# Performance work log

Measured on AMD Instinct MI355X. Metric: run time of the kernel, lower is better.

## Reference

```python
import jax, jax.numpy as jnp
import numpy as np

B, P, PLOIDY = 8, 5000, 2
NALLELES, NPOS, D = 16, 20000, 64


def setup_inputs() -> dict:
    key = jax.random.key(0)
    k1, k2, k3, k4, k5 = jax.random.split(key, 5)
    alleles = jax.random.randint(k1, (B, P, PLOIDY), 0, NALLELES, dtype=jnp.int32)
    positions = jax.random.randint(k2, (B, P), 0, NPOS, dtype=jnp.int32)
    allele_table = jax.random.normal(k3, (NALLELES, D), dtype=jnp.float32)
    kernel_table = jax.random.normal(k4, (NPOS, D * D), dtype=jnp.float32)
    bias_table = jax.random.normal(k5, (NPOS, D), dtype=jnp.float32)
    return {"alleles": alleles, "positions": positions,
            "allele_table": allele_table, "kernel_table": kernel_table,
            "bias_table": bias_table}


def reference(alleles, positions, allele_table, kernel_table, bias_table):
    # gather allele embeddings and sum over ploidy: [B,P,ploidy,D] -> [B,P,D]
    a = allele_table[alleles].sum(axis=-2)
    # per-position weight matrix: [B,P,D,D]
    kernel = kernel_table[positions].reshape(positions.shape[0], positions.shape[1], D, D)
    bias = bias_table[positions]                       # [B,P,D]
    # batched 1xD @ DxD matmul, fused with bias add
    out = jnp.einsum('bpd,bpde->bpe', a, kernel) + bias
    return out  # activation is None (linear)
```

## Files before the change

kernel.cpp:

```cpp
#include <hip/hip_runtime.h>

#define BB 8
#define PP 5000
#define DD 64
#define NBP (BB * PP)
#define NPOSC 20000
#define WAVES_PER_BLOCK 4
#define GRID_MAIN (NBP / WAVES_PER_BLOCK)

#define BSHIFT 4
#define NBUCKET 1250
#define NBUCKET_PAD 1280

__global__ __launch_bounds__(256) void hist_kernel(
    const int* __restrict__ positions, int* __restrict__ hist)
{
    const int tid = blockIdx.x * 256 + threadIdx.x;
    if (tid < NBP) atomicAdd(&hist[positions[tid] >> BSHIFT], 1);
}

__global__ __launch_bounds__(256) void scan_kernel(
    const int* __restrict__ hist, int* __restrict__ offs)
{
    __shared__ int lsum[256];
    const int t = threadIdx.x;
    const int base = t * 5;
    int v[5];
#pragma unroll
    for (int j = 0; j < 5; ++j)
        v[j] = (base + j < NBUCKET) ? hist[base + j] : 0;
    int run = 0;
#pragma unroll
    for (int j = 0; j < 5; ++j) { int x = v[j]; v[j] = run; run += x; }
    lsum[t] = run;
    __syncthreads();
    if (t == 0) {
        int acc = 0;
        for (int i = 0; i < 256; ++i) { int x = lsum[i]; lsum[i] = acc; acc += x; }
    }
    __syncthreads();
#pragma unroll
    for (int j = 0; j < 5; ++j)
        if (base + j < NBUCKET) offs[base + j] = lsum[t] + v[j];
}

__global__ __launch_bounds__(256) void scatter_kernel(
    const int* __restrict__ positions, int* __restrict__ offs,
    int* __restrict__ order)
{
    const int tid = blockIdx.x * 256 + threadIdx.x;
    if (tid < NBP) {
        const int b = positions[tid] >> BSHIFT;
        const int idx = atomicAdd(&offs[b], 1);
        order[idx] = tid;
    }
}

__global__ __launch_bounds__(256) void allele_embed_kernel(
    const int* __restrict__ alleles,
    const int* __restrict__ positions,
    const float* __restrict__ allele_table,
    const float4* __restrict__ ktab4,
    const float4* __restrict__ btab4,
    const int* __restrict__ order,
    float4* __restrict__ out4)
{
    const int wave = threadIdx.x >> 6;
    const int lane = threadIdx.x & 63;
    const int work = (blockIdx.x & 7) * (GRID_MAIN / 8) + (blockIdx.x >> 3);
    const int bp   = order[work * WAVES_PER_BLOCK + wave];

    const int al0 = alleles[bp * 2 + 0];
    const int al1 = alleles[bp * 2 + 1];
    const int pos = positions[bp];

    const float a_full = allele_table[al0 * DD + lane] + allele_table[al1 * DD + lane];

    const float4* __restrict__ krow = ktab4 + (size_t)pos * (DD * DD / 4);
    const int dg = lane >> 4;

    float4 acc = make_float4(0.f, 0.f, 0.f, 0.f);
#pragma unroll
    for (int i = 0; i < 16; ++i) {
        const int d    = i * 4 + dg;
        const float ad = __shfl(a_full, d, 64);
        const float4 kv = krow[i * 64 + lane];
        acc.x += ad * kv.x;
        acc.y += ad * kv.y;
        acc.z += ad * kv.z;
        acc.w += ad * kv.w;
    }

#pragma unroll
    for (int off = 16; off <= 32; off <<= 1) {
        acc.x += __shfl_xor(acc.x, off, 64);
        acc.y += __shfl_xor(acc.y, off, 64);
        acc.z += __shfl_xor(acc.z, off, 64);
        acc.w += __shfl_xor(acc.w, off, 64);
    }

    if (lane < 16) {
        const float4 bv = btab4[(size_t)pos * (DD / 4) + lane];
        acc.x += bv.x;
        acc.y += bv.y;
        acc.z += bv.z;
        acc.w += bv.w;
        out4[(size_t)bp * (DD / 4) + lane] = acc;
    }
}

extern "C" void kernel_launch(void* const* d_in, const int* in_sizes, int n_in,
                              void* d_out, int out_size, void* d_ws, size_t ws_size,
                              hipStream_t stream) {
    const int*   alleles      = (const int*)d_in[0];
    const int*   positions    = (const int*)d_in[1];
    const float* allele_table = (const float*)d_in[2];
    const float4* ktab4       = (const float4*)d_in[3];
    const float4* btab4       = (const float4*)d_in[4];
    float4* out4              = (float4*)d_out;

    int* hist  = (int*)d_ws;
    int* offs  = hist + NBUCKET_PAD;
    int* order = offs + NBUCKET_PAD;

    hipMemsetAsync(hist, 0, NBUCKET_PAD * sizeof(int), stream);

    const int gprep = (NBP + 255) / 256;
    hist_kernel<<<gprep, 256, 0, stream>>>(positions, hist);
    scan_kernel<<<1, 256, 0, stream>>>(hist, offs);
    scatter_kernel<<<gprep, 256, 0, stream>>>(positions, offs, order);

    allele_embed_kernel<<<GRID_MAIN, WAVES_PER_BLOCK * 64, 0, stream>>>(
        alleles, positions, allele_table, ktab4, btab4, order, out4);
}
```

Baseline: 452.4 us.

## Group items by exact position and reuse each kernel row across all its items

Measured after the change: 499.2 us. 1.1x slower.

```diff
diff --git a/kernel.cpp b/kernel.cpp
--- a/kernel.cpp
+++ b/kernel.cpp
@@ -5,107 +5,134 @@
 #define DD 64
 #define NBP (BB * PP)
 #define NPOSC 20000
-#define WAVES_PER_BLOCK 4
-#define GRID_MAIN (NBP / WAVES_PER_BLOCK)
+#define GRID_POS (NPOSC / 4)
+#define CHUNK 80
 
-#define BSHIFT 4
-#define NBUCKET 1250
-#define NBUCKET_PAD 1280
+static __device__ __forceinline__ float4 f4add(float4 a, float4 b) {
+    return make_float4(a.x + b.x, a.y + b.y, a.z + b.z, a.w + b.w);
+}
 
 __global__ __launch_bounds__(256) void hist_kernel(
     const int* __restrict__ positions, int* __restrict__ hist)
 {
     const int tid = blockIdx.x * 256 + threadIdx.x;
-    if (tid < NBP) atomicAdd(&hist[positions[tid] >> BSHIFT], 1);
+    if (tid < NBP) atomicAdd(&hist[positions[tid]], 1);
 }
 
 __global__ __launch_bounds__(256) void scan_kernel(
-    const int* __restrict__ hist, int* __restrict__ offs)
+    const int* __restrict__ hist, int* __restrict__ offs,
+    int* __restrict__ cursor)
 {
     __shared__ int lsum[256];
     const int t = threadIdx.x;
-    const int base = t * 5;
-    int v[5];
-#pragma unroll
-    for (int j = 0; j < 5; ++j)
-        v[j] = (base + j < NBUCKET) ? hist[base + j] : 0;
+    const int base = t * CHUNK;
     int run = 0;
-#pragma unroll
-    for (int j = 0; j < 5; ++j) { int x = v[j]; v[j] = run; run += x; }
+    for (int j = 0; j < CHUNK; ++j) {
+        const int idx = base + j;
+        if (idx < NPOSC) run += hist[idx];
+    }
     lsum[t] = run;
     __syncthreads();
     if (t == 0) {
         int acc = 0;
-        for (int i = 0; i < 256; ++i) { int x = lsum[i]; lsum[i] = acc; acc += x; }
+        for (int i = 0; i < 256; ++i) { const int x = lsum[i]; lsum[i] = acc; acc += x; }
     }
     __syncthreads();
-#pragma unroll
-    for (int j = 0; j < 5; ++j)
-        if (base + j < NBUCKET) offs[base + j] = lsum[t] + v[j];
+    int acc = lsum[t];
+    for (int j = 0; j < CHUNK; ++j) {
+        const int idx = base + j;
+        if (idx < NPOSC) {
+            offs[idx]   = acc;
+            cursor[idx] = acc;
+            acc += hist[idx];
+        }
+    }
+    if (t == 255) offs[NPOSC] = acc;
 }
 
 __global__ __launch_bounds__(256) void scatter_kernel(
-    const int* __restrict__ positions, int* __restrict__ offs,
+    const int* __restrict__ positions, int* __restrict__ cursor,
     int* __restrict__ order)
 {
     const int tid = blockIdx.x * 256 + threadIdx.x;
     if (tid < NBP) {
-        const int b = positions[tid] >> BSHIFT;
-        const int idx = atomicAdd(&offs[b], 1);
+        const int idx = atomicAdd(&cursor[positions[tid]], 1);
         order[idx] = tid;
     }
 }
 
 __global__ __launch_bounds__(256) void allele_embed_kernel(
     const int* __restrict__ alleles,
-    const int* __restrict__ positions,
     const float* __restrict__ allele_table,
     const float4* __restrict__ ktab4,
     const float4* __restrict__ btab4,
+    const int* __restrict__ offs,
     const int* __restrict__ order,
     float4* __restrict__ out4)
 {
     const int wave = threadIdx.x >> 6;
     const int lane = threadIdx.x & 63;
-    const int work = (blockIdx.x & 7) * (GRID_MAIN / 8) + (blockIdx.x >> 3);
-    const int bp   = order[work * WAVES_PER_BLOCK + wave];
+    const int work = (blockIdx.x & 7) * (GRID_POS / 8) + (blockIdx.x >> 3);
+    const int pos  = work * 4 + wave;
 
-    const int al0 = alleles[bp * 2 + 0];
-    const int al1 = alleles[bp * 2 + 1];
-    const int pos = positions[bp];
-
-    const float a_full = allele_table[al0 * DD + lane] + allele_table[al1 * DD + lane];
+    const int start = offs[pos];
+    const int end   = offs[pos + 1];
+    if (start == end) return;
 
     const float4* __restrict__ krow = ktab4 + (size_t)pos * (DD * DD / 4);
     const int dg = lane >> 4;
+    const float4 bv = btab4[(size_t)pos * (DD / 4) + (lane & 15)];
 
-    float4 acc = make_float4(0.f, 0.f, 0.f, 0.f);
+    for (int c = start; c < end; c += 4) {
+        const int m = end - c;
+        const int bp0 = order[c];
+        const int bp1 = (m > 1) ? order[c + 1] : bp0;
+        const int bp2 = (m > 2) ? order[c + 2] : bp0;
+        const int bp3 = (m > 3) ? order[c + 3] : bp0;
+
+        const float a0 = allele_table[alleles[bp0 * 2] * DD + lane]
+                       + allele_table[alleles[bp0 * 2 + 1] * DD + lane];
+        const float a1 = allele_table[alleles[bp1 * 2] * DD + lane]
+                       + allele_table[alleles[bp1 * 2 + 1] * DD + lane];
+        const float a2 = allele_table[alleles[bp2 * 2] * DD + lane]
+                       + allele_table[alleles[bp2 * 2 + 1] * DD + lane];
+        const float a3 = allele_table[alleles[bp3 * 2] * DD + lane]
+                       + allele_table[alleles[bp3 * 2 + 1] * DD + lane];
+
+        float4 acc0 = make_float4(0.f, 0.f, 0.f, 0.f);
+        float4 acc1 = acc0, acc2 = acc0, acc3 = acc0;
 #pragma unroll
-    for (int i = 0; i < 16; ++i) {
-        const int d    = i * 4 + dg;
-        const float ad = __shfl(a_full, d, 64);
-        const float4 kv = krow[i * 64 + lane];
-        acc.x += ad * kv.x;
-        acc.y += ad * kv.y;
-        acc.z += ad * kv.z;
-        acc.w += ad * kv.w;
-    }
+        for (int i = 0; i < 16; ++i) {
+            const int d = i * 4 + dg;
+            const float4 kv = krow[i * 64 + lane];
+            const float d0 = __shfl(a0, d, 64);
+            const float d1 = __shfl(a1, d, 64);
+            const float d2 = __shfl(a2, d, 64);
+            const float d3 = __shfl(a3, d, 64);
+            acc0.x += d0 * kv.x; acc0.y += d0 * kv.y; acc0.z += d0 * kv.z; acc0.w += d0 * kv.w;
+            acc1.x += d1 * kv.x; acc1.y += d1 * kv.y; acc1.z += d1 * kv.z; acc1.w += d1 * kv.w;
+            acc2.x += d2 * kv.x; acc2.y += d2 * kv.y; acc2.z += d2 * kv.z; acc2.w += d2 * kv.w;
+            acc3.x += d3 * kv.x; acc3.y += d3 * kv.y; acc3.z += d3 * kv.z; acc3.w += d3 * kv.w;
+        }
 
 #pragma unroll
-    for (int off = 16; off <= 32; off <<= 1) {
-        acc.x += __shfl_xor(acc.x, off, 64);
-        acc.y += __shfl_xor(acc.y, off, 64);
-        acc.z += __shfl_xor(acc.z, off, 64);
-        acc.w += __shfl_xor(acc.w, off, 64);
-    }
+        for (int off = 16; off <= 32; off <<= 1) {
+            acc0.x += __shfl_xor(acc0.x, off, 64); acc0.y += __shfl_xor(acc0.y, off, 64);
+            acc0.z += __shfl_xor(acc0.z, off, 64); acc0.w += __shfl_xor(acc0.w, off, 64);
+            acc1.x += __shfl_xor(acc1.x, off, 64); acc1.y += __shfl_xor(acc1.y, off, 64);
+            acc1.z += __shfl_xor(acc1.z, off, 64); acc1.w += __shfl_xor(acc1.w, off, 64);
+            acc2.x += __shfl_xor(acc2.x, off, 64); acc2.y += __shfl_xor(acc2.y, off, 64);
+            acc2.z += __shfl_xor(acc2.z, off, 64); acc2.w += __shfl_xor(acc2.w, off, 64);
+            acc3.x += __shfl_xor(acc3.x, off, 64); acc3.y += __shfl_xor(acc3.y, off, 64);
+            acc3.z += __shfl_xor(acc3.z, off, 64); acc3.w += __shfl_xor(acc3.w, off, 64);
+        }
 
-    if (lane < 16) {
-        const float4 bv = btab4[(size_t)pos * (DD / 4) + lane];
-        acc.x += bv.x;
-        acc.y += bv.y;
-        acc.z += bv.z;
-        acc.w += bv.w;
-        out4[(size_t)bp * (DD / 4) + lane] = acc;
+        if (lane < 16) {
+            out4[(size_t)bp0 * (DD / 4) + lane] = f4add(acc0, bv);
+            if (m > 1) out4[(size_t)bp1 * (DD / 4) + lane] = f4add(acc1, bv);
+            if (m > 2) out4[(size_t)bp2 * (DD / 4) + lane] = f4add(acc2, bv);
+            if (m > 3) out4[(size_t)bp3 * (DD / 4) + lane] = f4add(acc3, bv);
+        }
     }
 }
 
@@ -119,17 +146,18 @@
     const float4* btab4       = (const float4*)d_in[4];
     float4* out4              = (float4*)d_out;
 
-    int* hist  = (int*)d_ws;
-    int* offs  = hist + NBUCKET_PAD;
-    int* order = offs + NBUCKET_PAD;
+    int* hist   = (int*)d_ws;
+    int* offs   = hist + NPOSC;
+    int* cursor = offs + (NPOSC + 1);
+    int* order  = cursor + NPOSC;
 
-    hipMemsetAsync(hist, 0, NBUCKET_PAD * sizeof(int), stream);
+    hipMemsetAsync(hist, 0, NPOSC * sizeof(int), stream);
 
     const int gprep = (NBP + 255) / 256;
     hist_kernel<<<gprep, 256, 0, stream>>>(positions, hist);
-    scan_kernel<<<1, 256, 0, stream>>>(hist, offs);
-    scatter_kernel<<<gprep, 256, 0, stream>>>(positions, offs, order);
+    scan_kernel<<<1, 256, 0, stream>>>(hist, offs, cursor);
+    scatter_kernel<<<gprep, 256, 0, stream>>>(positions, cursor, order);
 
-    allele_embed_kernel<<<GRID_MAIN, WAVES_PER_BLOCK * 64, 0, stream>>>(
-        alleles, positions, allele_table, ktab4, btab4, order, out4);
+    allele_embed_kernel<<<GRID_POS, 256, 0, stream>>>(
+        alleles, allele_table, ktab4, btab4, offs, order, out4);
 }
```
